# Kernel optimization log

Measured on AMD Instinct MI355X. Metric: run time of the kernel, lower is better.

The kernel has to match this reference:

```python
import jax, jax.numpy as jnp
import numpy as np

B, IN, NC, O, H = 256, 2048, 1000, 4096, 4  # batch, in_features, num_classes, n_decoders, hidden
NEG_SLOPE = 0.1

def setup_inputs() -> dict:
    key = jax.random.key(0)
    ks = jax.random.split(key, 7)
    s1 = 1.0 / np.sqrt(IN)
    s2 = 1.0 / np.sqrt(H)
    return {
        "x":   jax.random.normal(ks[0], (B, IN), jnp.float32),
        "fcW": jax.random.normal(ks[1], (NC, IN), jnp.float32) * s1,
        "fcb": jax.random.normal(ks[2], (NC,), jnp.float32) * s1,
        "W1":  jax.random.normal(ks[3], (O, IN, H), jnp.float32) * s1,
        "b1":  jax.random.normal(ks[4], (O, H), jnp.float32) * s1,
        "W2":  jax.random.normal(ks[5], (O, H), jnp.float32) * s2,
        "b2":  jax.random.normal(ks[6], (O,), jnp.float32) * s2,
    }

def reference(x, fcW, fcb, W1, b1, W2, b2):
    # fc head: x1 = x @ fcW^T + fcb  -> [B, NC]
    x1 = jnp.einsum("bi,ci->bc", x, fcW) + fcb
    # 4096 tiny MLPs batched into one grouped GEMM:
    # h = leaky_relu(x @ W1_o + b1_o) for each decoder o  -> [B, O, H]
    h = jnp.einsum("bi,oih->boh", x, W1) + b1
    h = jnp.where(h >= 0, h, NEG_SLOPE * h)
    # second layer (H->1) collapses to a weighted reduction -> [B, O]
    x2 = jnp.einsum("boh,oh->bo", h, W2) + b2
    return (x1, x2)
```

## Files before the change

### kernel.cpp

```cpp
#include <hip/hip_runtime.h>


typedef __bf16 bf16_t;
typedef __bf16 bf16x4 __attribute__((ext_vector_type(4)));
typedef __bf16 bf16x8 __attribute__((ext_vector_type(8)));
typedef float  f32x4  __attribute__((ext_vector_type(4)));
typedef float  f32x16 __attribute__((ext_vector_type(16)));

#define GLDS(gp, lp) __builtin_amdgcn_global_load_lds( \
    (const __attribute__((address_space(1))) void*)(gp), \
    (__attribute__((address_space(3))) void*)(lp), 16, 0, 0)

#define WS_A_OFF 0
#define WS_F_OFF (64 * 16384)

__global__ __launch_bounds__(256)
void pack_tiles(const float* __restrict__ x, const float* __restrict__ fcW,
                char* __restrict__ ws)
{
    const int tid = threadIdx.x;
    const int bid = blockIdx.x;
    if (bid < 64) {
        const int rg = bid >> 5, kt = bid & 31;
        char* dst = ws + WS_A_OFF + (size_t)bid * 16384;
        #pragma unroll
        for (int i = 0; i < 4; ++i) {
            const int gi = tid + 256 * i;
            const int r = gi >> 3, s = gi & 7, g = s ^ (r & 7);
            const float* sp = x + (size_t)(rg * 128 + r) * 2048 + kt * 64 + g * 8;
            f32x4 v0 = *(const f32x4*)sp, v1 = *(const f32x4*)(sp + 4);
            bf16x8 o;
            #pragma unroll
            for (int c = 0; c < 4; ++c) { o[c] = (bf16_t)v0[c]; o[4 + c] = (bf16_t)v1[c]; }
            *(bf16x8*)(dst + r * 128 + s * 16) = o;
        }
    } else {
        const int t = bid - 64;
        const int cg = t >> 5, kt = t & 31;
        char* dst = ws + WS_F_OFF + (size_t)t * 8192;
        #pragma unroll
        for (int i = 0; i < 2; ++i) {
            const int gi = tid + 256 * i;
            const int n = gi >> 3, s = gi & 7, g = s ^ ((n >> 2) & 7);
            const int c = cg * 64 + n;
            bf16x8 o;
            if (c < 1000) {
                const float* sp = fcW + (size_t)c * 2048 + kt * 64 + g * 8;
                f32x4 v0 = *(const f32x4*)sp, v1 = *(const f32x4*)(sp + 4);
                #pragma unroll
                for (int cc = 0; cc < 4; ++cc) { o[cc] = (bf16_t)v0[cc]; o[4 + cc] = (bf16_t)v1[cc]; }
            } else {
                #pragma unroll
                for (int cc = 0; cc < 8; ++cc) o[cc] = (bf16_t)0.f;
            }
            *(bf16x8*)(dst + n * 128 + s * 16) = o;
        }
    }
}

__global__ __launch_bounds__(256, 3)
void fused_dual(const char* __restrict__ ws,
                const float* __restrict__ W1,
                const float* __restrict__ fcb,
                const float* __restrict__ b1,
                const float* __restrict__ W2,
                const float* __restrict__ b2,
                float* __restrict__ out)
{
    __shared__ __align__(16) char lds[2][24576];

    const int tid  = threadIdx.x;
    const int lane = tid & 63, w = tid >> 6;
    const int l31  = lane & 31, half = lane >> 5;

    const int idx = blockIdx.x;
    const int wid = (idx & 7) * 68 + (idx >> 3);
    const int cg  = wid >> 1, rg = wid & 1, m0 = rg * 128;
    const bool is_fc = (cg < 16);
    const int c0  = (is_fc ? cg : cg - 16) * 64;
    const int dcg = is_fc ? 0 : (cg - 16);

    const char* aT = ws + WS_A_OFF + (size_t)rg * 32 * 16384;
    const char* bT = ws + WS_F_OFF + (size_t)cg * 32 * 8192;

    const int lo = lane * 16;

    const int u    = tid & 127, hi = tid >> 7;
    const int oloc = u >> 3, gg = u & 7;
    const int slot = gg ^ (oloc & 7);
    const float* w1Base = W1 + (size_t)(dcg * 16 + oloc) * 8192
                             + (gg * 8 + hi * 4) * 4;
    const int wbase = (4 * oloc) * 128 + slot * 16 + hi * 8;

    f32x4 bReg[4];

    auto B_LOAD = [&](int kt) {
        const float* p = w1Base + kt * 256;
        #pragma unroll
        for (int j = 0; j < 4; ++j) bReg[j] = *(const f32x4*)(p + j * 4);
    };
    auto B_WRITE = [&](int pbuf) {
        char* lB = &lds[pbuf][16384];
        #pragma unroll
        for (int h = 0; h < 4; ++h) {
            bf16x4 v;
            #pragma unroll
            for (int j = 0; j < 4; ++j) v[j] = (bf16_t)bReg[j][h];
            *(bf16x4*)(lB + wbase + h * 128) = v;
        }
    };
    auto GLDS_A = [&](int kt, int pbuf) {
        char* lA = &lds[pbuf][0];
        const char* ga = aT + kt * 16384 + w * 4096;
        #pragma unroll
        for (int i = 0; i < 4; ++i)
            GLDS(ga + i * 1024 + lo, lA + w * 4096 + i * 1024);
    };
    auto GLDS_B_FC = [&](int kt, int pbuf) {
        char* lB = &lds[pbuf][16384];
        const char* gb = bT + kt * 8192 + w * 2048;
        #pragma unroll
        for (int i = 0; i < 2; ++i)
            GLDS(gb + i * 1024 + lo, lB + w * 2048 + i * 1024);
    };

    const int mh = (w & 1) * 64, nh = (w >> 1) * 32;
    f32x16 acc[2];
    #pragma unroll
    for (int i = 0; i < 2; ++i)
        #pragma unroll
        for (int r = 0; r < 16; ++r) acc[i][r] = 0.f;

    if (is_fc) {
        GLDS_A(0, 0); GLDS_B_FC(0, 0);
    } else {
        B_LOAD(0); GLDS_A(0, 0); B_WRITE(0);
    }
    __syncthreads();

    const int nrow = nh + l31;
    const int bro  = nrow * 128 + (((nrow >> 2) & 7) << 4);
    for (int kt = 0; kt < 32; ++kt) {
        const int p = kt & 1;
        if (kt < 31) {
            if (is_fc) { GLDS_A(kt + 1, p ^ 1); GLDS_B_FC(kt + 1, p ^ 1); }
            else       { B_LOAD(kt + 1); GLDS_A(kt + 1, p ^ 1); }
        }
        const char* lA = &lds[p][0];
        const char* lB = &lds[p][16384];
        #pragma unroll
        for (int ks = 0; ks < 4; ++ks) {
            const int g = ks * 2 + half;
            bf16x8 bf = *(const bf16x8*)(lB + (bro ^ (g << 4)));
            #pragma unroll
            for (int i = 0; i < 2; ++i) {
                const int mrow = mh + i * 32 + l31;
                bf16x8 af = *(const bf16x8*)(lA + mrow * 128 + ((g ^ (mrow & 7)) << 4));
                acc[i] = __builtin_amdgcn_mfma_f32_32x32x16_bf16(af, bf, acc[i], 0, 0, 0);
            }
        }
        if (!is_fc && kt < 31) B_WRITE(p ^ 1);
        __syncthreads();
    }

    if (is_fc) {
        const int c = c0 + nh + l31;
        if (c < 1000) {
            const float bias = fcb[c];
            #pragma unroll
            for (int i = 0; i < 2; ++i)
            #pragma unroll
            for (int r = 0; r < 16; ++r) {
                const int m = m0 + mh + i * 32 + (r & 3) + 8 * (r >> 2) + 4 * half;
                out[m * 1000 + c] = acc[i][r] + bias;
            }
        }
    } else {
        float* x2 = out + 256 * 1000;
        const int d = cg - 16;
        const int n_glob = c0 + nh + l31;
        const float b1v = b1[n_glob], w2v = W2[n_glob];
        const float b2v = b2[n_glob >> 2];
        float* xs = (float*)lds;
        const int o_loc = (nh + l31) >> 2;
        #pragma unroll
        for (int i = 0; i < 2; ++i)
        #pragma unroll
        for (int r = 0; r < 16; ++r) {
            float h = acc[i][r] + b1v;
            h = (h >= 0.f) ? h : 0.1f * h;
            float wv = h * w2v;
            wv += __shfl_xor(wv, 1, 64);
            wv += __shfl_xor(wv, 2, 64);
            if ((lane & 3) == 0) {
                const int row = mh + i * 32 + (r & 3) + 8 * (r >> 2) + 4 * half;
                xs[row * 16 + o_loc] = wv + b2v;
            }
        }
        __syncthreads();
        #pragma unroll
        for (int j = 0; j < 2; ++j) {
            const int row = (tid >> 2) + 64 * j, part = tid & 3;
            f32x4 v = *(const f32x4*)(xs + row * 16 + part * 4);
            *(f32x4*)(x2 + (m0 + row) * 4096 + d * 16 + part * 4) = v;
        }
    }
}

extern "C" void kernel_launch(void* const* d_in, const int* in_sizes, int n_in,
                              void* d_out, int out_size, void* d_ws, size_t ws_size,
                              hipStream_t stream)
{
    (void)in_sizes; (void)n_in; (void)out_size; (void)ws_size;
    const float* x   = (const float*)d_in[0];
    const float* fcW = (const float*)d_in[1];
    const float* fcb = (const float*)d_in[2];
    const float* W1  = (const float*)d_in[3];
    const float* b1  = (const float*)d_in[4];
    const float* W2  = (const float*)d_in[5];
    const float* b2  = (const float*)d_in[6];
    char* ws = (char*)d_ws;
    pack_tiles<<<576, 256, 0, stream>>>(x, fcW, ws);
    fused_dual<<<544, 256, 0, stream>>>(ws, W1, fcb, b1, W2, b2, (float*)d_out);
}
```

Measured before the change: 254.7 us.

## Halve row tile to 64 with 128-thread blocks and doubled grid

Each workgroup of the fused GEMM kernel now covers 64 batch rows with two waves instead of 128 rows with four waves, and the grid doubles to 1088 blocks. Each wave now loads one A fragment per k-step and reuses it across two B fragments, and W1 staging loads eight float4s per thread to write bf16x8 into LDS. The intent is more blocks to spread across CUs, less LDS per block, and wider LDS writes. It also raises instruction priority around the MFMA loop. The cost is that every W1 column group is loaded and converted twice as often, since two blocks now share each column group, and fewer waves per block are available to hide latency.

```diff
diff --git a/kernel.cpp b/kernel.cpp
--- a/kernel.cpp
+++ b/kernel.cpp
@@ -2,7 +2,6 @@
 
 
 typedef __bf16 bf16_t;
-typedef __bf16 bf16x4 __attribute__((ext_vector_type(4)));
 typedef __bf16 bf16x8 __attribute__((ext_vector_type(8)));
 typedef float  f32x4  __attribute__((ext_vector_type(4)));
 typedef float  f32x16 __attribute__((ext_vector_type(16)));
@@ -58,7 +57,7 @@
     }
 }
 
-__global__ __launch_bounds__(256, 3)
+__global__ __launch_bounds__(128, 2)
 void fused_dual(const char* __restrict__ ws,
                 const float* __restrict__ W1,
                 const float* __restrict__ fcb,
@@ -67,64 +66,61 @@
                 const float* __restrict__ b2,
                 float* __restrict__ out)
 {
-    __shared__ __align__(16) char lds[2][24576];
+    __shared__ __align__(16) char lds[2][16384];
 
     const int tid  = threadIdx.x;
     const int lane = tid & 63, w = tid >> 6;
     const int l31  = lane & 31, half = lane >> 5;
 
     const int idx = blockIdx.x;
-    const int wid = (idx & 7) * 68 + (idx >> 3);
-    const int cg  = wid >> 1, rg = wid & 1, m0 = rg * 128;
+    const int wid = (idx & 7) * 136 + (idx >> 3);
+    const int cg  = wid >> 2, rg = wid & 3, m0 = rg * 64;
     const bool is_fc = (cg < 16);
     const int c0  = (is_fc ? cg : cg - 16) * 64;
     const int dcg = is_fc ? 0 : (cg - 16);
 
-    const char* aT = ws + WS_A_OFF + (size_t)rg * 32 * 16384;
+    const char* aT = ws + WS_A_OFF + (size_t)(rg >> 1) * 32 * 16384 + (rg & 1) * 8192;
     const char* bT = ws + WS_F_OFF + (size_t)cg * 32 * 8192;
 
     const int lo = lane * 16;
 
-    const int u    = tid & 127, hi = tid >> 7;
-    const int oloc = u >> 3, gg = u & 7;
-    const int slot = gg ^ (oloc & 7);
-    const float* w1Base = W1 + (size_t)(dcg * 16 + oloc) * 8192
-                             + (gg * 8 + hi * 4) * 4;
-    const int wbase = (4 * oloc) * 128 + slot * 16 + hi * 8;
-
-    f32x4 bReg[4];
+    const int oloc = tid >> 3, gg = tid & 7;
+    const float* w1Base = W1 + (size_t)(dcg * 16 + oloc) * 8192 + gg * 32;
+    const int wbase = (4 * oloc) * 128 + (gg ^ (oloc & 7)) * 16;
+
+    f32x4 bReg[8];
 
     auto B_LOAD = [&](int kt) {
         const float* p = w1Base + kt * 256;
         #pragma unroll
-        for (int j = 0; j < 4; ++j) bReg[j] = *(const f32x4*)(p + j * 4);
+        for (int j = 0; j < 8; ++j) bReg[j] = *(const f32x4*)(p + j * 4);
     };
     auto B_WRITE = [&](int pbuf) {
-        char* lB = &lds[pbuf][16384];
+        char* lB = &lds[pbuf][8192];
         #pragma unroll
         for (int h = 0; h < 4; ++h) {
-            bf16x4 v;
-            #pragma unroll
-            for (int j = 0; j < 4; ++j) v[j] = (bf16_t)bReg[j][h];
-            *(bf16x4*)(lB + wbase + h * 128) = v;
+            bf16x8 v;
+            #pragma unroll
+            for (int j = 0; j < 8; ++j) v[j] = (bf16_t)bReg[j][h];
+            *(bf16x8*)(lB + wbase + h * 128) = v;
         }
     };
     auto GLDS_A = [&](int kt, int pbuf) {
         char* lA = &lds[pbuf][0];
-        const char* ga = aT + kt * 16384 + w * 4096;
+        const char* ga = aT + (size_t)kt * 16384 + w * 4096;
         #pragma unroll
         for (int i = 0; i < 4; ++i)
             GLDS(ga + i * 1024 + lo, lA + w * 4096 + i * 1024);
     };
     auto GLDS_B_FC = [&](int kt, int pbuf) {
-        char* lB = &lds[pbuf][16384];
-        const char* gb = bT + kt * 8192 + w * 2048;
-        #pragma unroll
-        for (int i = 0; i < 2; ++i)
-            GLDS(gb + i * 1024 + lo, lB + w * 2048 + i * 1024);
-    };
-
-    const int mh = (w & 1) * 64, nh = (w >> 1) * 32;
+        char* lB = &lds[pbuf][8192];
+        const char* gb = bT + (size_t)kt * 8192 + w * 4096;
+        #pragma unroll
+        for (int i = 0; i < 4; ++i)
+            GLDS(gb + i * 1024 + lo, lB + w * 4096 + i * 1024);
+    };
+
+    const int mh = w * 32;
     f32x16 acc[2];
     #pragma unroll
     for (int i = 0; i < 2; ++i)
@@ -138,8 +134,7 @@
     }
     __syncthreads();
 
-    const int nrow = nh + l31;
-    const int bro  = nrow * 128 + (((nrow >> 2) & 7) << 4);
+    const int mrow = mh + l31;
     for (int kt = 0; kt < 32; ++kt) {
         const int p = kt & 1;
         if (kt < 31) {
@@ -147,60 +142,64 @@
             else       { B_LOAD(kt + 1); GLDS_A(kt + 1, p ^ 1); }
         }
         const char* lA = &lds[p][0];
-        const char* lB = &lds[p][16384];
+        const char* lB = &lds[p][8192];
+        __builtin_amdgcn_s_setprio(1);
         #pragma unroll
         for (int ks = 0; ks < 4; ++ks) {
             const int g = ks * 2 + half;
-            bf16x8 bf = *(const bf16x8*)(lB + (bro ^ (g << 4)));
+            bf16x8 af = *(const bf16x8*)(lA + mrow * 128 + ((g ^ (mrow & 7)) << 4));
             #pragma unroll
             for (int i = 0; i < 2; ++i) {
-                const int mrow = mh + i * 32 + l31;
-                bf16x8 af = *(const bf16x8*)(lA + mrow * 128 + ((g ^ (mrow & 7)) << 4));
+                const int nrow = i * 32 + l31;
+                bf16x8 bf = *(const bf16x8*)(lB + nrow * 128 + ((g ^ ((nrow >> 2) & 7)) << 4));
                 acc[i] = __builtin_amdgcn_mfma_f32_32x32x16_bf16(af, bf, acc[i], 0, 0, 0);
             }
         }
+        __builtin_amdgcn_s_setprio(0);
         if (!is_fc && kt < 31) B_WRITE(p ^ 1);
         __syncthreads();
     }
 
     if (is_fc) {
-        const int c = c0 + nh + l31;
-        if (c < 1000) {
-            const float bias = fcb[c];
-            #pragma unroll
-            for (int i = 0; i < 2; ++i)
-            #pragma unroll
-            for (int r = 0; r < 16; ++r) {
-                const int m = m0 + mh + i * 32 + (r & 3) + 8 * (r >> 2) + 4 * half;
-                out[m * 1000 + c] = acc[i][r] + bias;
+        #pragma unroll
+        for (int i = 0; i < 2; ++i) {
+            const int c = c0 + i * 32 + l31;
+            if (c < 1000) {
+                const float bias = fcb[c];
+                #pragma unroll
+                for (int r = 0; r < 16; ++r) {
+                    const int m = m0 + mh + (r & 3) + 8 * (r >> 2) + 4 * half;
+                    out[m * 1000 + c] = acc[i][r] + bias;
+                }
             }
         }
     } else {
         float* x2 = out + 256 * 1000;
         const int d = cg - 16;
-        const int n_glob = c0 + nh + l31;
-        const float b1v = b1[n_glob], w2v = W2[n_glob];
-        const float b2v = b2[n_glob >> 2];
         float* xs = (float*)lds;
-        const int o_loc = (nh + l31) >> 2;
-        #pragma unroll
-        for (int i = 0; i < 2; ++i)
-        #pragma unroll
-        for (int r = 0; r < 16; ++r) {
-            float h = acc[i][r] + b1v;
-            h = (h >= 0.f) ? h : 0.1f * h;
-            float wv = h * w2v;
-            wv += __shfl_xor(wv, 1, 64);
-            wv += __shfl_xor(wv, 2, 64);
-            if ((lane & 3) == 0) {
-                const int row = mh + i * 32 + (r & 3) + 8 * (r >> 2) + 4 * half;
-                xs[row * 16 + o_loc] = wv + b2v;
+        #pragma unroll
+        for (int i = 0; i < 2; ++i) {
+            const int n_glob = c0 + i * 32 + l31;
+            const float b1v = b1[n_glob], w2v = W2[n_glob];
+            const float b2v = b2[n_glob >> 2];
+            const int o_loc = (i * 32 + l31) >> 2;
+            #pragma unroll
+            for (int r = 0; r < 16; ++r) {
+                float h = acc[i][r] + b1v;
+                h = (h >= 0.f) ? h : 0.1f * h;
+                float wv = h * w2v;
+                wv += __shfl_xor(wv, 1, 64);
+                wv += __shfl_xor(wv, 2, 64);
+                if ((lane & 3) == 0) {
+                    const int row = mh + (r & 3) + 8 * (r >> 2) + 4 * half;
+                    xs[row * 16 + o_loc] = wv + b2v;
+                }
             }
         }
         __syncthreads();
         #pragma unroll
         for (int j = 0; j < 2; ++j) {
-            const int row = (tid >> 2) + 64 * j, part = tid & 3;
+            const int row = (tid >> 2) + 32 * j, part = tid & 3;
             f32x4 v = *(const f32x4*)(xs + row * 16 + part * 4);
             *(f32x4*)(x2 + (m0 + row) * 4096 + d * 16 + part * 4) = v;
         }
@@ -221,5 +220,5 @@
     const float* b2  = (const float*)d_in[6];
     char* ws = (char*)d_ws;
     pack_tiles<<<576, 256, 0, stream>>>(x, fcW, ws);
-    fused_dual<<<544, 256, 0, stream>>>(ws, W1, fcb, b1, W2, b2, (float*)d_out);
+    fused_dual<<<1088, 128, 0, stream>>>(ws, W1, fcb, b1, W2, b2, (float*)d_out);
 }
```

Result: slower. 278.1 us (+9.2%).

## Restructure fused GEMM: full-M tiles with resident B in 128KB LDS

Applied to the files above, without the earlier changes.

Each workgroup now covers all 256 batch rows and a 32-column slice. It loads half the K dimension of its B tile (W1 converted to bf16, or packed fcW) into a large LDS buffer in one go, then streams double-buffered A tiles through, with a custom vmcnt wait and barrier. W1 is read once per decoder group instead of twice across row groups, and the per-iteration B conversion stall is removed. The cost is one workgroup per CU from the 128KB LDS. The fcW packing swizzle changes to match the new B row layout, and the grid becomes 512 decoder blocks plus 32 fc blocks.

```diff
diff --git a/kernel.cpp b/kernel.cpp
--- a/kernel.cpp
+++ b/kernel.cpp
@@ -2,7 +2,6 @@
 
 
 typedef __bf16 bf16_t;
-typedef __bf16 bf16x4 __attribute__((ext_vector_type(4)));
 typedef __bf16 bf16x8 __attribute__((ext_vector_type(8)));
 typedef float  f32x4  __attribute__((ext_vector_type(4)));
 typedef float  f32x16 __attribute__((ext_vector_type(16)));
@@ -41,7 +40,7 @@
         #pragma unroll
         for (int i = 0; i < 2; ++i) {
             const int gi = tid + 256 * i;
-            const int n = gi >> 3, s = gi & 7, g = s ^ ((n >> 2) & 7);
+            const int n = gi >> 3, s = gi & 7, g = s ^ (n & 7);
             const int c = cg * 64 + n;
             bf16x8 o;
             if (c < 1000) {
@@ -58,7 +57,7 @@
     }
 }
 
-__global__ __launch_bounds__(256, 3)
+__global__ __launch_bounds__(256, 1)
 void fused_dual(const char* __restrict__ ws,
                 const float* __restrict__ W1,
                 const float* __restrict__ fcb,
@@ -67,122 +66,117 @@
                 const float* __restrict__ b2,
                 float* __restrict__ out)
 {
-    __shared__ __align__(16) char lds[2][24576];
+    __shared__ __align__(16) char lds[131072];
+    char* lB = lds;
 
     const int tid  = threadIdx.x;
     const int lane = tid & 63, w = tid >> 6;
     const int l31  = lane & 31, half = lane >> 5;
 
     const int idx = blockIdx.x;
-    const int wid = (idx & 7) * 68 + (idx >> 3);
-    const int cg  = wid >> 1, rg = wid & 1, m0 = rg * 128;
-    const bool is_fc = (cg < 16);
-    const int c0  = (is_fc ? cg : cg - 16) * 64;
-    const int dcg = is_fc ? 0 : (cg - 16);
-
-    const char* aT = ws + WS_A_OFF + (size_t)rg * 32 * 16384;
-    const char* bT = ws + WS_F_OFF + (size_t)cg * 32 * 8192;
-
-    const int lo = lane * 16;
-
-    const int u    = tid & 127, hi = tid >> 7;
-    const int oloc = u >> 3, gg = u & 7;
-    const int slot = gg ^ (oloc & 7);
-    const float* w1Base = W1 + (size_t)(dcg * 16 + oloc) * 8192
-                             + (gg * 8 + hi * 4) * 4;
-    const int wbase = (4 * oloc) * 128 + slot * 16 + hi * 8;
-
-    f32x4 bReg[4];
-
-    auto B_LOAD = [&](int kt) {
-        const float* p = w1Base + kt * 256;
-        #pragma unroll
-        for (int j = 0; j < 4; ++j) bReg[j] = *(const f32x4*)(p + j * 4);
+    const int wid = (idx < 512) ? ((idx & 7) * 64 + (idx >> 3)) : idx;
+    const bool is_fc = (wid >= 512);
+    const int d   = wid;
+    const int fcI = wid - 512;
+
+    const int o_loc = tid & 7;
+    const float* w1o = W1 + (size_t)(d * 8 + o_loc) * 8192;
+    const int cbase = (tid >> 3) * 4;
+
+    const int cgo = fcI >> 1, rowhalf = fcI & 1;
+    const char* fcSrc = ws + WS_F_OFF + (size_t)cgo * 32 * 8192 + rowhalf * 4096;
+
+    f32x4 rga[8], rgb[8];
+    auto BL = [&](int kh, int r, f32x4* R) {
+        const float* p = w1o + kh * 4096 + (cbase + r) * 32;
+        #pragma unroll
+        for (int j = 0; j < 8; ++j) R[j] = *(const f32x4*)(p + j * 4);
     };
-    auto B_WRITE = [&](int pbuf) {
-        char* lB = &lds[pbuf][16384];
+    auto BW = [&](int r, const f32x4* R) {
+        const int idxk = cbase + r;
+        const int ktl = idxk >> 3, g = idxk & 7;
+        char* base = lB + ktl * 4096 + (4 * o_loc) * 128;
         #pragma unroll
         for (int h = 0; h < 4; ++h) {
-            bf16x4 v;
-            #pragma unroll
-            for (int j = 0; j < 4; ++j) v[j] = (bf16_t)bReg[j][h];
-            *(bf16x4*)(lB + wbase + h * 128) = v;
+            bf16x8 v;
+            #pragma unroll
+            for (int j = 0; j < 8; ++j) v[j] = (bf16_t)R[j][h];
+            const int n7 = (4 * o_loc + h) & 7;
+            *(bf16x8*)(base + h * 128 + ((g ^ n7) << 4)) = v;
         }
     };
-    auto GLDS_A = [&](int kt, int pbuf) {
-        char* lA = &lds[pbuf][0];
-        const char* ga = aT + kt * 16384 + w * 4096;
-        #pragma unroll
-        for (int i = 0; i < 4; ++i)
-            GLDS(ga + i * 1024 + lo, lA + w * 4096 + i * 1024);
+
+    auto GLDS_A = [&](int ktg, int pbuf) {
+        char* dst = lds + 65536 + pbuf * 32768 + w * 8192;
+        const char* src = ws + WS_A_OFF + (size_t)(w >> 1) * 524288
+                        + (size_t)ktg * 16384 + (w & 1) * 8192 + lane * 16;
+        #pragma unroll
+        for (int i = 0; i < 8; ++i)
+            GLDS(src + i * 1024, dst + i * 1024);
     };
-    auto GLDS_B_FC = [&](int kt, int pbuf) {
-        char* lB = &lds[pbuf][16384];
-        const char* gb = bT + kt * 8192 + w * 2048;
-        #pragma unroll
-        for (int i = 0; i < 2; ++i)
-            GLDS(gb + i * 1024 + lo, lB + w * 2048 + i * 1024);
-    };
-
-    const int mh = (w & 1) * 64, nh = (w >> 1) * 32;
+
     f32x16 acc[2];
     #pragma unroll
     for (int i = 0; i < 2; ++i)
         #pragma unroll
         for (int r = 0; r < 16; ++r) acc[i][r] = 0.f;
 
+    for (int kh = 0; kh < 2; ++kh) {
+        if (is_fc) {
+            #pragma unroll
+            for (int ktl = 0; ktl < 16; ++ktl)
+                GLDS(fcSrc + (size_t)(kh * 16 + ktl) * 8192 + w * 1024 + lane * 16,
+                     lB + ktl * 4096 + w * 1024);
+        } else {
+            BL(kh, 0, rga); BL(kh, 1, rgb);
+            BW(0, rga);     BL(kh, 2, rga);
+            BW(1, rgb);     BL(kh, 3, rgb);
+            BW(2, rga);     BW(3, rgb);
+        }
+        GLDS_A(kh * 16, 0);
+        __syncthreads();
+
+        for (int ktl = 0; ktl < 16; ++ktl) {
+            const int p = ktl & 1;
+            if (ktl < 15) GLDS_A(kh * 16 + ktl + 1, p ^ 1);
+            const char* A  = lds + 65536 + p * 32768;
+            const char* Bt = lB + ktl * 4096;
+            #pragma unroll
+            for (int ks = 0; ks < 4; ++ks) {
+                const int g = ks * 2 + half;
+                bf16x8 bf = *(const bf16x8*)(Bt + l31 * 128 + ((g ^ (l31 & 7)) << 4));
+                #pragma unroll
+                for (int i = 0; i < 2; ++i) {
+                    const int mrow = w * 64 + i * 32 + l31;
+                    bf16x8 af = *(const bf16x8*)(A + mrow * 128 + ((g ^ (mrow & 7)) << 4));
+                    acc[i] = __builtin_amdgcn_mfma_f32_32x32x16_bf16(af, bf, acc[i], 0, 0, 0);
+                }
+            }
+            asm volatile("s_waitcnt vmcnt(0)" ::: "memory");
+            __builtin_amdgcn_s_barrier();
+            asm volatile("" ::: "memory");
+        }
+    }
+
     if (is_fc) {
-        GLDS_A(0, 0); GLDS_B_FC(0, 0);
-    } else {
-        B_LOAD(0); GLDS_A(0, 0); B_WRITE(0);
-    }
-    __syncthreads();
-
-    const int nrow = nh + l31;
-    const int bro  = nrow * 128 + (((nrow >> 2) & 7) << 4);
-    for (int kt = 0; kt < 32; ++kt) {
-        const int p = kt & 1;
-        if (kt < 31) {
-            if (is_fc) { GLDS_A(kt + 1, p ^ 1); GLDS_B_FC(kt + 1, p ^ 1); }
-            else       { B_LOAD(kt + 1); GLDS_A(kt + 1, p ^ 1); }
-        }
-        const char* lA = &lds[p][0];
-        const char* lB = &lds[p][16384];
-        #pragma unroll
-        for (int ks = 0; ks < 4; ++ks) {
-            const int g = ks * 2 + half;
-            bf16x8 bf = *(const bf16x8*)(lB + (bro ^ (g << 4)));
-            #pragma unroll
-            for (int i = 0; i < 2; ++i) {
-                const int mrow = mh + i * 32 + l31;
-                bf16x8 af = *(const bf16x8*)(lA + mrow * 128 + ((g ^ (mrow & 7)) << 4));
-                acc[i] = __builtin_amdgcn_mfma_f32_32x32x16_bf16(af, bf, acc[i], 0, 0, 0);
-            }
-        }
-        if (!is_fc && kt < 31) B_WRITE(p ^ 1);
-        __syncthreads();
-    }
-
-    if (is_fc) {
-        const int c = c0 + nh + l31;
+        const int c = fcI * 32 + l31;
         if (c < 1000) {
             const float bias = fcb[c];
             #pragma unroll
             for (int i = 0; i < 2; ++i)
             #pragma unroll
             for (int r = 0; r < 16; ++r) {
-                const int m = m0 + mh + i * 32 + (r & 3) + 8 * (r >> 2) + 4 * half;
+                const int m = w * 64 + i * 32 + (r & 3) + 8 * (r >> 2) + 4 * half;
                 out[m * 1000 + c] = acc[i][r] + bias;
             }
         }
     } else {
         float* x2 = out + 256 * 1000;
-        const int d = cg - 16;
-        const int n_glob = c0 + nh + l31;
+        const int n_glob = d * 32 + l31;
         const float b1v = b1[n_glob], w2v = W2[n_glob];
         const float b2v = b2[n_glob >> 2];
-        float* xs = (float*)lds;
-        const int o_loc = (nh + l31) >> 2;
+        float* xs = (float*)(lds + 65536);
+        const int o8 = l31 >> 2;
         #pragma unroll
         for (int i = 0; i < 2; ++i)
         #pragma unroll
@@ -193,16 +187,16 @@
             wv += __shfl_xor(wv, 1, 64);
             wv += __shfl_xor(wv, 2, 64);
             if ((lane & 3) == 0) {
-                const int row = mh + i * 32 + (r & 3) + 8 * (r >> 2) + 4 * half;
-                xs[row * 16 + o_loc] = wv + b2v;
+                const int row = w * 64 + i * 32 + (r & 3) + 8 * (r >> 2) + 4 * half;
+                xs[row * 8 + o8] = wv + b2v;
             }
         }
         __syncthreads();
         #pragma unroll
         for (int j = 0; j < 2; ++j) {
-            const int row = (tid >> 2) + 64 * j, part = tid & 3;
-            f32x4 v = *(const f32x4*)(xs + row * 16 + part * 4);
-            *(f32x4*)(x2 + (m0 + row) * 4096 + d * 16 + part * 4) = v;
+            const int row = (tid >> 1) + j * 128, part = tid & 1;
+            f32x4 v = *(const f32x4*)(xs + row * 8 + part * 4);
+            *(f32x4*)(x2 + (size_t)row * 4096 + d * 8 + part * 4) = v;
         }
     }
 }
```

Result: slower. 267.3 us (+4.9%).
